# Kernel optimization log

Measured on AMD Instinct MI355X. Metric: run time of the kernel, lower is better.

## Reference

```python
import jax, jax.numpy as jnp
import numpy as np

HEADS = 4
OUT = 64  # hidden_channels


def gat_conv(x, src, dst, N, W, att_src, att_dst, bias):
    # x: [N, Fin] -> h: [N, H, C]
    h = (x @ W).reshape(N, HEADS, OUT)
    a_s = (h * att_src).sum(-1)  # [N, H]
    a_d = (h * att_dst).sum(-1)  # [N, H]
    logits = jax.nn.leaky_relu(a_s[src] + a_d[dst], negative_slope=0.2)  # [E, H]
    # segment softmax over incoming edges of each destination node
    m = jax.ops.segment_max(logits, dst, num_segments=N)
    e = jnp.exp(logits - m[dst])
    z = jax.ops.segment_sum(e, dst, num_segments=N)
    alpha = e / (z[dst] + 1e-16)
    out = jax.ops.segment_sum(h[src] * alpha[:, :, None], dst, num_segments=N)
    return out.reshape(N, HEADS * OUT) + bias


def setup_inputs() -> dict:
    key = jax.random.key(0)
    ks = jax.random.split(key, 16)
    N, E, F = 50000, 800000, 128
    HC = HEADS * OUT  # 256
    s = 0.1
    return {
        "x": jax.random.normal(ks[0], (N, F), jnp.float32),
        "edge_index": jax.random.randint(ks[1], (2, E), 0, N, dtype=jnp.int32),
        "W1": jax.random.normal(ks[2], (F, HC), jnp.float32) * s,
        "as1": jax.random.normal(ks[3], (1, HEADS, OUT), jnp.float32) * s,
        "ad1": jax.random.normal(ks[4], (1, HEADS, OUT), jnp.float32) * s,
        "b1": jnp.zeros((HC,), jnp.float32),
        "W2": jax.random.normal(ks[5], (HC, HC), jnp.float32) * s,
        "as2": jax.random.normal(ks[6], (1, HEADS, OUT), jnp.float32) * s,
        "ad2": jax.random.normal(ks[7], (1, HEADS, OUT), jnp.float32) * s,
        "b2": jnp.zeros((HC,), jnp.float32),
        "lw1": jax.random.normal(ks[8], (HC, OUT), jnp.float32) * s,
        "lb1": jnp.zeros((OUT,), jnp.float32),
        "lw2": jax.random.normal(ks[9], (OUT, 2), jnp.float32) * s,
        "lb2": jnp.zeros((2,), jnp.float32),
    }


def reference(x, edge_index, W1, as1, ad1, b1, W2, as2, ad2, b2, lw1, lb1, lw2, lb2):
    N = x.shape[0]
    # PyG GATConv default add_self_loops=True
    loop = jnp.arange(N, dtype=edge_index.dtype)
    src = jnp.concatenate([edge_index[0], loop])
    dst = jnp.concatenate([edge_index[1], loop])
    h = jax.nn.elu(gat_conv(x, src, dst, N, W1, as1, ad1, b1))
    # dropout is identity at inference
    h = jax.nn.elu(gat_conv(h, src, dst, N, W2, as2, ad2, b2))
    h = jax.nn.relu(h @ lw1 + lb1)
    return jax.nn.log_softmax(h @ lw2 + lb2, axis=1)
```

## Files before the change

kernel.cpp:

```cpp
#include <hip/hip_runtime.h>
#include <math.h>


typedef __attribute__((ext_vector_type(8))) _Float16 half8v;
typedef __attribute__((ext_vector_type(4))) float f32x4;

__device__ __forceinline__ float lrelu(float x) { return x > 0.f ? x : 0.2f * x; }
__device__ __forceinline__ float elu1(float x) { return x > 0.f ? x : (__expf(x) - 1.f); }

__global__ void convert_weights_kernel(const float* __restrict__ W1, const float* __restrict__ W2,
                                       const float* __restrict__ lw1,
                                       _Float16* __restrict__ o1, _Float16* __restrict__ o2,
                                       _Float16* __restrict__ o3, int* __restrict__ indeg,
                                       int N) {
  int t = blockIdx.x * blockDim.x + threadIdx.x;
  if (t < 32768) {
    int n = t >> 7, k = t & 127;
    o1[t] = (_Float16)W1[(long)k * 256 + n];
  } else if (t < 98304) {
    int i = t - 32768;
    int n = i >> 8, k = i & 255;
    o2[i] = (_Float16)W2[(long)k * 256 + n];
  } else if (t < 114688) {
    int i = t - 98304;
    int n = i >> 8, k = i & 255;
    o3[i] = (_Float16)lw1[(long)k * 64 + n];
  } else if (t < 114688 + N) {
    indeg[t - 114688] = 0;
  }
}

__global__ void count_kernel(const int* __restrict__ dst, int E, int* __restrict__ indeg) {
  int e = blockIdx.x * blockDim.x + threadIdx.x;
  if (e < E) atomicAdd(&indeg[dst[e]], 1);
}

__global__ void scan_block_kernel(const int* __restrict__ in, int* __restrict__ incl,
                                  int* __restrict__ bsum, int N) {
  __shared__ int wsum[16];
  int gid = blockIdx.x * 1024 + threadIdx.x;
  int lane = threadIdx.x & 63, w = threadIdx.x >> 6;
  int v = (gid < N) ? in[gid] : 0;
  int sv = v;
#pragma unroll
  for (int o = 1; o < 64; o <<= 1) {
    int t = __shfl_up(sv, o);
    if (lane >= o) sv += t;
  }
  if (lane == 63) wsum[w] = sv;
  __syncthreads();
  if (w == 0) {
    int bs = (lane < 16) ? wsum[lane] : 0;
#pragma unroll
    for (int o = 1; o < 16; o <<= 1) {
      int t = __shfl_up(bs, o);
      if (lane >= o) bs += t;
    }
    if (lane < 16) wsum[lane] = bs;
  }
  __syncthreads();
  if (w > 0) sv += wsum[w - 1];
  if (gid < N) incl[gid] = sv;
  if (threadIdx.x == 1023) bsum[blockIdx.x] = sv;
}

__global__ void scan_finalize_kernel(const int* __restrict__ in, const int* __restrict__ incl,
                                     const int* __restrict__ bsum, int* __restrict__ off,
                                     int* __restrict__ cursor, int N) {
  int gid = blockIdx.x * blockDim.x + threadIdx.x;
  if (gid >= N) return;
  int b = gid >> 10;
  int carry = 0;
  for (int k = 0; k < b; ++k) carry += bsum[k];
  int ic = incl[gid] + carry;
  off[gid + 1] = ic;
  cursor[gid] = ic - in[gid];
  if (gid == 0) off[0] = 0;
}

__global__ void fill_kernel(const int* __restrict__ src, const int* __restrict__ dst, int E,
                            int* __restrict__ cursor, int* __restrict__ csr_src) {
  int e = blockIdx.x * blockDim.x + threadIdx.x;
  if (e < E) {
    int pos = atomicAdd(&cursor[dst[e]], 1);
    csr_src[pos] = src[e];
  }
}

template <typename AT>
__launch_bounds__(256)
__global__ void mfma_gemm_attn_kernel(const AT* __restrict__ A,
                                      const _Float16* __restrict__ B,
                                      const float* __restrict__ att_s,
                                      const float* __restrict__ att_d,
                                      _Float16* __restrict__ C,
                                      float* __restrict__ a_s, float* __restrict__ a_d,
                                      int M, int K) {
  __shared__ _Float16 As[64][40];
  __shared__ _Float16 Bs[2][64][40];
  int tid = threadIdx.x;
  int bm = blockIdx.y * 64, bn = blockIdx.x * 128;
  int lane = tid & 63, wave = tid >> 6;
  int srow = tid >> 2, sch = (tid & 3) * 8;
  const AT* Ap = A + (long)(bm + srow) * K + sch;
  const _Float16* Bp0 = B + (long)(bn + srow) * K + sch;
  const _Float16* Bp1 = B + (long)(bn + 64 + srow) * K + sch;
  bool arow_ok = (bm + srow) < M;
  int fm = lane & 15, fq = lane >> 4;
  f32x4 acc[2][4];
#pragma unroll
  for (int t = 0; t < 2; ++t)
#pragma unroll
    for (int cb = 0; cb < 4; ++cb) acc[t][cb] = (f32x4){0.f, 0.f, 0.f, 0.f};
  for (int k0 = 0; k0 < K; k0 += 32) {
    half8v a8 = {0, 0, 0, 0, 0, 0, 0, 0};
    if (arow_ok) {
      if constexpr (sizeof(AT) == 4) {
        float4 f0 = *(const float4*)(Ap + k0);
        float4 f1 = *(const float4*)(Ap + k0 + 4);
        a8 = (half8v){(_Float16)f0.x, (_Float16)f0.y, (_Float16)f0.z, (_Float16)f0.w,
                      (_Float16)f1.x, (_Float16)f1.y, (_Float16)f1.z, (_Float16)f1.w};
      } else {
        a8 = *(const half8v*)(Ap + k0);
      }
    }
    uint4 vb0 = *(const uint4*)(Bp0 + k0);
    uint4 vb1 = *(const uint4*)(Bp1 + k0);
    *(half8v*)&As[srow][sch] = a8;
    *(uint4*)&Bs[0][srow][sch] = vb0;
    *(uint4*)&Bs[1][srow][sch] = vb1;
    __syncthreads();
    half8v ah = *(const half8v*)&As[wave * 16 + fm][fq * 8];
#pragma unroll
    for (int t = 0; t < 2; ++t)
#pragma unroll
      for (int cb = 0; cb < 4; ++cb) {
        half8v bh = *(const half8v*)&Bs[t][cb * 16 + fm][fq * 8];
        acc[t][cb] = __builtin_amdgcn_mfma_f32_16x16x32_f16(ah, bh, acc[t][cb], 0, 0, 0);
      }
    __syncthreads();
  }
  int row0 = bm + wave * 16 + fq * 4;
#pragma unroll
  for (int t = 0; t < 2; ++t) {
    int headi = blockIdx.x * 2 + t;
    int cbase = bn + t * 64;
    float asv[4], adv[4];
#pragma unroll
    for (int cb = 0; cb < 4; ++cb) {
      int col = cbase + cb * 16 + fm;
      asv[cb] = att_s[col];
      adv[cb] = att_d[col];
    }
#pragma unroll
    for (int r = 0; r < 4; ++r) {
      int row = row0 + r;
      float sp = 0.f, dp = 0.f;
#pragma unroll
      for (int cb = 0; cb < 4; ++cb) {
        float v = acc[t][cb][r];
        sp = fmaf(v, asv[cb], sp);
        dp = fmaf(v, adv[cb], dp);
        if (row < M) C[(long)row * 256 + cbase + cb * 16 + fm] = (_Float16)v;
      }
#pragma unroll
      for (int o = 1; o < 16; o <<= 1) {
        sp += __shfl_xor(sp, o);
        dp += __shfl_xor(dp, o);
      }
      if (fm == 0 && row < M) {
        a_s[(long)row * 4 + headi] = sp;
        a_d[(long)row * 4 + headi] = dp;
      }
    }
  }
}

__launch_bounds__(256)
__global__ void head_mfma_kernel(const _Float16* __restrict__ A, const _Float16* __restrict__ B,
                                 const float* __restrict__ lb1, const float* __restrict__ lw2,
                                 const float* __restrict__ lb2, float* __restrict__ out, int M) {
  __shared__ _Float16 As[64][40];
  __shared__ _Float16 Bs[64][40];
  int tid = threadIdx.x;
  int bm = blockIdx.x * 64;
  int lane = tid & 63, wave = tid >> 6;
  int srow = tid >> 2, sch = (tid & 3) * 8;
  const _Float16* Ap = A + (long)(bm + srow) * 256 + sch;
  const _Float16* Bp = B + (long)srow * 256 + sch;
  int fm = lane & 15, fq = lane >> 4;
  f32x4 acc[4];
#pragma unroll
  for (int cb = 0; cb < 4; ++cb) acc[cb] = (f32x4){0.f, 0.f, 0.f, 0.f};
  for (int k0 = 0; k0 < 256; k0 += 32) {
    uint4 va = *(const uint4*)(Ap + k0);
    uint4 vb = *(const uint4*)(Bp + k0);
    *(uint4*)&As[srow][sch] = va;
    *(uint4*)&Bs[srow][sch] = vb;
    __syncthreads();
    half8v ah = *(const half8v*)&As[wave * 16 + fm][fq * 8];
#pragma unroll
    for (int cb = 0; cb < 4; ++cb) {
      half8v bh = *(const half8v*)&Bs[cb * 16 + fm][fq * 8];
      acc[cb] = __builtin_amdgcn_mfma_f32_16x16x32_f16(ah, bh, acc[cb], 0, 0, 0);
    }
    __syncthreads();
  }
  float lb1c[4], w20[4], w21[4];
#pragma unroll
  for (int cb = 0; cb < 4; ++cb) {
    int col = cb * 16 + fm;
    lb1c[cb] = lb1[col];
    w20[cb] = lw2[col * 2 + 0];
    w21[cb] = lw2[col * 2 + 1];
  }
  float b20 = lb2[0], b21 = lb2[1];
#pragma unroll
  for (int r = 0; r < 4; ++r) {
    float v0 = 0.f, v1 = 0.f;
#pragma unroll
    for (int cb = 0; cb < 4; ++cb) {
      float s = fmaxf(acc[cb][r] + lb1c[cb], 0.f);
      v0 = fmaf(s, w20[cb], v0);
      v1 = fmaf(s, w21[cb], v1);
    }
#pragma unroll
    for (int o = 1; o < 16; o <<= 1) {
      v0 += __shfl_xor(v0, o);
      v1 += __shfl_xor(v1, o);
    }
    if (fm == 0) {
      int row = bm + wave * 16 + fq * 4 + r;
      if (row < M) {
        v0 += b20;
        v1 += b21;
        float mx = fmaxf(v0, v1);
        float ls = mx + logf(expf(v0 - mx) + expf(v1 - mx));
        out[(long)row * 2 + 0] = v0 - ls;
        out[(long)row * 2 + 1] = v1 - ls;
      }
    }
  }
}

__launch_bounds__(256)
__global__ void gat_aggregate8_kernel(const _Float16* __restrict__ h,
                                      const float* __restrict__ a_s,
                                      const float* __restrict__ a_d,
                                      const int* __restrict__ off,
                                      const int* __restrict__ csr_src,
                                      const float* __restrict__ bias,
                                      _Float16* __restrict__ outp, int N) {
  int wid = (blockIdx.x * blockDim.x + threadIdx.x) >> 6;
  int lane = threadIdx.x & 63;
  if (wid >= N) return;
  int c = lane & 31, hlf = lane >> 5, head4 = c >> 3;
  int h1 = lane & 3, sl1 = lane >> 2;
  int beg = off[wid], cnt = off[wid + 1] - beg;
  float ad_h1 = a_d[wid * 4 + h1];
  float m = lrelu(a_s[wid * 4 + h1] + ad_h1);
  float acc[8] = {};
  float z = 0.f;
  if (hlf == 0) {
    z = 1.f;
    half8v sr = *(const half8v*)(h + (long)wid * 256 + c * 8);
#pragma unroll
    for (int i = 0; i < 8; ++i) acc[i] = (float)sr[i];
  }
  for (int c0 = 0; c0 < cnt; c0 += 16) {
    int i2 = c0 + (lane & 15);
    int sv = (i2 < cnt) ? csr_src[beg + i2] : 0;
    int i1 = c0 + sl1;
    int spi = __shfl(sv, sl1);
    float l = (i1 < cnt) ? lrelu(a_s[(long)spi * 4 + h1] + ad_h1) : -1e30f;
    float lm = l;
    lm = fmaxf(lm, __shfl_xor(lm, 4));
    lm = fmaxf(lm, __shfl_xor(lm, 8));
    lm = fmaxf(lm, __shfl_xor(lm, 16));
    lm = fmaxf(lm, __shfl_xor(lm, 32));
    float m_new = fmaxf(m, lm);
    float alpha = __expf(m - m_new);
    float pv = (i1 < cnt) ? __expf(l - m_new) : 0.f;
    m = m_new;
    float alpha4 = __shfl(alpha, head4);
    z *= alpha4;
#pragma unroll
    for (int i = 0; i < 8; ++i) acc[i] *= alpha4;
#pragma unroll 4
    for (int j = 0; j < 16; j += 2) {
      if (c0 + j >= cnt) break;
      int e = j + hlf;
      int s = __shfl(sv, e);
      float p = __shfl(pv, e * 4 + head4);
      z += p;
      half8v rv = *(const half8v*)(h + (long)s * 256 + c * 8);
      acc[0] = fmaf(p, (float)rv[0], acc[0]);
      acc[1] = fmaf(p, (float)rv[1], acc[1]);
      acc[2] = fmaf(p, (float)rv[2], acc[2]);
      acc[3] = fmaf(p, (float)rv[3], acc[3]);
      acc[4] = fmaf(p, (float)rv[4], acc[4]);
      acc[5] = fmaf(p, (float)rv[5], acc[5]);
      acc[6] = fmaf(p, (float)rv[6], acc[6]);
      acc[7] = fmaf(p, (float)rv[7], acc[7]);
    }
  }
  z += __shfl_xor(z, 32);
#pragma unroll
  for (int i = 0; i < 8; ++i) acc[i] += __shfl_xor(acc[i], 32);
  if (hlf == 0) {
    float inv = 1.f / z;
    half8v o;
#pragma unroll
    for (int i = 0; i < 8; ++i) o[i] = (_Float16)elu1(fmaf(acc[i], inv, bias[c * 8 + i]));
    *(half8v*)(outp + (long)wid * 256 + c * 8) = o;
  }
}

static inline int cdiv(int a, int b) { return (a + b - 1) / b; }

extern "C" void kernel_launch(void* const* d_in, const int* in_sizes, int n_in,
                              void* d_out, int out_size, void* d_ws, size_t ws_size,
                              hipStream_t stream) {
  const float* x = (const float*)d_in[0];
  const int* ei = (const int*)d_in[1];
  const float* W1 = (const float*)d_in[2];
  const float* as1 = (const float*)d_in[3];
  const float* ad1 = (const float*)d_in[4];
  const float* b1 = (const float*)d_in[5];
  const float* W2 = (const float*)d_in[6];
  const float* as2 = (const float*)d_in[7];
  const float* ad2 = (const float*)d_in[8];
  const float* b2 = (const float*)d_in[9];
  const float* lw1 = (const float*)d_in[10];
  const float* lb1 = (const float*)d_in[11];
  const float* lw2 = (const float*)d_in[12];
  const float* lb2 = (const float*)d_in[13];
  float* out = (float*)d_out;

  int N = in_sizes[0] / 128;
  int E = in_sizes[1] / 2;
  int Mp = cdiv(N, 64) * 64;

  char* ws = (char*)d_ws;
  _Float16* Wt1 = (_Float16*)ws; ws += 256 * 128 * 2;
  _Float16* Wt2 = (_Float16*)ws; ws += 256 * 256 * 2;
  _Float16* WL = (_Float16*)ws; ws += 64 * 256 * 2;
  _Float16* C = (_Float16*)ws; ws += (size_t)Mp * 256 * 2;
  _Float16* h2 = (_Float16*)ws; ws += (size_t)Mp * 256 * 2;
  float* aS = (float*)ws; ws += (size_t)N * 4 * 4;
  float* aD = (float*)ws; ws += (size_t)N * 4 * 4;
  int* csr_src = (int*)ws; ws += (size_t)E * 4;
  int* indeg = (int*)ws; ws += (size_t)N * 4;
  int* cursor = (int*)ws; ws += (size_t)N * 4;
  int* off = (int*)ws; ws += (size_t)(N + 4) * 4;
  int* incl = (int*)ws; ws += (size_t)N * 4;
  int* bsum = (int*)ws; ws += 64 * 4;

  const int* e_src = ei;
  const int* e_dst = ei + E;
  int nb = cdiv(N, 1024);

  convert_weights_kernel<<<cdiv(114688 + N, 256), 256, 0, stream>>>(W1, W2, lw1, Wt1, Wt2, WL,
                                                                    indeg, N);

  count_kernel<<<cdiv(E, 256), 256, 0, stream>>>(e_dst, E, indeg);
  scan_block_kernel<<<nb, 1024, 0, stream>>>(indeg, incl, bsum, N);
  scan_finalize_kernel<<<cdiv(N, 256), 256, 0, stream>>>(indeg, incl, bsum, off, cursor, N);
  fill_kernel<<<cdiv(E, 256), 256, 0, stream>>>(e_src, e_dst, E, cursor, csr_src);

  mfma_gemm_attn_kernel<float><<<dim3(2, Mp / 64), 256, 0, stream>>>(x, Wt1, as1, ad1, C, aS, aD,
                                                                     N, 128);
  gat_aggregate8_kernel<<<cdiv(N, 4), 256, 0, stream>>>(C, aS, aD, off, csr_src, b1, h2, N);

  mfma_gemm_attn_kernel<_Float16><<<dim3(2, Mp / 64), 256, 0, stream>>>(h2, Wt2, as2, ad2, C, aS,
                                                                        aD, N, 256);
  gat_aggregate8_kernel<<<cdiv(N, 4), 256, 0, stream>>>(C, aS, aD, off, csr_src, b2, h2, N);

  head_mfma_kernel<<<Mp / 64, 256, 0, stream>>>(h2, WL, lb1, lw2, lb2, out, N);
}
```

Baseline: 362.4 us.

## Store features in column-slice blocks and split aggregation into stats and sliced passes

```diff
diff --git a/kernel.cpp b/kernel.cpp
--- a/kernel.cpp
+++ b/kernel.cpp
@@ -95,14 +95,19 @@
                                       const float* __restrict__ att_d,
                                       _Float16* __restrict__ C,
                                       float* __restrict__ a_s, float* __restrict__ a_d,
-                                      int M, int K) {
+                                      int M, int K, int Mp) {
   __shared__ _Float16 As[64][40];
   __shared__ _Float16 Bs[2][64][40];
   int tid = threadIdx.x;
   int bm = blockIdx.y * 64, bn = blockIdx.x * 128;
   int lane = tid & 63, wave = tid >> 6;
   int srow = tid >> 2, sch = (tid & 3) * 8;
-  const AT* Ap = A + (long)(bm + srow) * K + sch;
+  const AT* Ap;
+  if constexpr (sizeof(AT) == 4) {
+    Ap = A + (long)(bm + srow) * K + sch;
+  } else {
+    Ap = A + (long)(bm + srow) * 32 + sch;
+  }
   const _Float16* Bp0 = B + (long)(bn + srow) * K + sch;
   const _Float16* Bp1 = B + (long)(bn + 64 + srow) * K + sch;
   bool arow_ok = (bm + srow) < M;
@@ -121,7 +126,7 @@
         a8 = (half8v){(_Float16)f0.x, (_Float16)f0.y, (_Float16)f0.z, (_Float16)f0.w,
                       (_Float16)f1.x, (_Float16)f1.y, (_Float16)f1.z, (_Float16)f1.w};
       } else {
-        a8 = *(const half8v*)(Ap + k0);
+        a8 = *(const half8v*)(Ap + (long)(k0 >> 5) * Mp * 32);
       }
     }
     uint4 vb0 = *(const uint4*)(Bp0 + k0);
@@ -161,7 +166,10 @@
         float v = acc[t][cb][r];
         sp = fmaf(v, asv[cb], sp);
         dp = fmaf(v, adv[cb], dp);
-        if (row < M) C[(long)row * 256 + cbase + cb * 16 + fm] = (_Float16)v;
+        if (row < M) {
+          int col = cbase + cb * 16 + fm;
+          C[((long)(col >> 5) * Mp + row) * 32 + (col & 31)] = (_Float16)v;
+        }
       }
 #pragma unroll
       for (int o = 1; o < 16; o <<= 1) {
@@ -179,21 +187,22 @@
 __launch_bounds__(256)
 __global__ void head_mfma_kernel(const _Float16* __restrict__ A, const _Float16* __restrict__ B,
                                  const float* __restrict__ lb1, const float* __restrict__ lw2,
-                                 const float* __restrict__ lb2, float* __restrict__ out, int M) {
+                                 const float* __restrict__ lb2, float* __restrict__ out,
+                                 int M, int Mp) {
   __shared__ _Float16 As[64][40];
   __shared__ _Float16 Bs[64][40];
   int tid = threadIdx.x;
   int bm = blockIdx.x * 64;
   int lane = tid & 63, wave = tid >> 6;
   int srow = tid >> 2, sch = (tid & 3) * 8;
-  const _Float16* Ap = A + (long)(bm + srow) * 256 + sch;
+  const _Float16* Ap = A + (long)(bm + srow) * 32 + sch;
   const _Float16* Bp = B + (long)srow * 256 + sch;
   int fm = lane & 15, fq = lane >> 4;
   f32x4 acc[4];
 #pragma unroll
   for (int cb = 0; cb < 4; ++cb) acc[cb] = (f32x4){0.f, 0.f, 0.f, 0.f};
   for (int k0 = 0; k0 < 256; k0 += 32) {
-    uint4 va = *(const uint4*)(Ap + k0);
+    uint4 va = *(const uint4*)(Ap + (long)(k0 >> 5) * Mp * 32);
     uint4 vb = *(const uint4*)(Bp + k0);
     *(uint4*)&As[srow][sch] = va;
     *(uint4*)&Bs[srow][sch] = vb;
@@ -244,75 +253,99 @@
 }
 
 __launch_bounds__(256)
-__global__ void gat_aggregate8_kernel(const _Float16* __restrict__ h,
-                                      const float* __restrict__ a_s,
-                                      const float* __restrict__ a_d,
-                                      const int* __restrict__ off,
-                                      const int* __restrict__ csr_src,
-                                      const float* __restrict__ bias,
-                                      _Float16* __restrict__ outp, int N) {
+__global__ void attn_softmax_stats_kernel(const float* __restrict__ a_s,
+                                          const float* __restrict__ a_d,
+                                          const int* __restrict__ off,
+                                          const int* __restrict__ csr_src,
+                                          float* __restrict__ mOut,
+                                          float* __restrict__ zInvOut, int N) {
   int wid = (blockIdx.x * blockDim.x + threadIdx.x) >> 6;
   int lane = threadIdx.x & 63;
   if (wid >= N) return;
-  int c = lane & 31, hlf = lane >> 5, head4 = c >> 3;
-  int h1 = lane & 3, sl1 = lane >> 2;
+  int h1 = lane & 3, slot = lane >> 2;
   int beg = off[wid], cnt = off[wid + 1] - beg;
   float ad_h1 = a_d[wid * 4 + h1];
   float m = lrelu(a_s[wid * 4 + h1] + ad_h1);
-  float acc[8] = {};
-  float z = 0.f;
-  if (hlf == 0) {
-    z = 1.f;
-    half8v sr = *(const half8v*)(h + (long)wid * 256 + c * 8);
-#pragma unroll
-    for (int i = 0; i < 8; ++i) acc[i] = (float)sr[i];
-  }
+  float z = (slot == 0) ? 1.f : 0.f;
   for (int c0 = 0; c0 < cnt; c0 += 16) {
-    int i2 = c0 + (lane & 15);
-    int sv = (i2 < cnt) ? csr_src[beg + i2] : 0;
-    int i1 = c0 + sl1;
-    int spi = __shfl(sv, sl1);
-    float l = (i1 < cnt) ? lrelu(a_s[(long)spi * 4 + h1] + ad_h1) : -1e30f;
+    int i = c0 + slot;
+    int sv = (i < cnt) ? csr_src[beg + i] : 0;
+    float l = (i < cnt) ? lrelu(a_s[(long)sv * 4 + h1] + ad_h1) : -1e30f;
     float lm = l;
     lm = fmaxf(lm, __shfl_xor(lm, 4));
     lm = fmaxf(lm, __shfl_xor(lm, 8));
     lm = fmaxf(lm, __shfl_xor(lm, 16));
     lm = fmaxf(lm, __shfl_xor(lm, 32));
     float m_new = fmaxf(m, lm);
-    float alpha = __expf(m - m_new);
-    float pv = (i1 < cnt) ? __expf(l - m_new) : 0.f;
+    z *= __expf(m - m_new);
+    z += (i < cnt) ? __expf(l - m_new) : 0.f;
     m = m_new;
-    float alpha4 = __shfl(alpha, head4);
-    z *= alpha4;
-#pragma unroll
-    for (int i = 0; i < 8; ++i) acc[i] *= alpha4;
-#pragma unroll 4
-    for (int j = 0; j < 16; j += 2) {
-      if (c0 + j >= cnt) break;
-      int e = j + hlf;
-      int s = __shfl(sv, e);
-      float p = __shfl(pv, e * 4 + head4);
-      z += p;
-      half8v rv = *(const half8v*)(h + (long)s * 256 + c * 8);
-      acc[0] = fmaf(p, (float)rv[0], acc[0]);
-      acc[1] = fmaf(p, (float)rv[1], acc[1]);
-      acc[2] = fmaf(p, (float)rv[2], acc[2]);
-      acc[3] = fmaf(p, (float)rv[3], acc[3]);
-      acc[4] = fmaf(p, (float)rv[4], acc[4]);
-      acc[5] = fmaf(p, (float)rv[5], acc[5]);
-      acc[6] = fmaf(p, (float)rv[6], acc[6]);
-      acc[7] = fmaf(p, (float)rv[7], acc[7]);
-    }
-  }
+  }
+  z += __shfl_xor(z, 4);
+  z += __shfl_xor(z, 8);
+  z += __shfl_xor(z, 16);
   z += __shfl_xor(z, 32);
-#pragma unroll
-  for (int i = 0; i < 8; ++i) acc[i] += __shfl_xor(acc[i], 32);
-  if (hlf == 0) {
-    float inv = 1.f / z;
+  if (slot == 0) {
+    mOut[(long)h1 * N + wid] = m;
+    zInvOut[(long)h1 * N + wid] = 1.f / (z + 1e-16f);
+  }
+}
+
+__launch_bounds__(256)
+__global__ void gat_aggregate_slice_kernel(const _Float16* __restrict__ hblk,
+                                           const float* __restrict__ a_s,
+                                           const float* __restrict__ a_d,
+                                           const float* __restrict__ mArr,
+                                           const float* __restrict__ zInv,
+                                           const int* __restrict__ off,
+                                           const int* __restrict__ csr_src,
+                                           const float* __restrict__ bias,
+                                           _Float16* __restrict__ outblk,
+                                           int N, int Mp) {
+  int bid = blockIdx.x;
+  int slice = bid & 7;
+  int wid = (bid >> 3) * 4 + (threadIdx.x >> 6);
+  int lane = threadIdx.x & 63;
+  if (wid >= N) return;
+  int colg = lane & 3, slot = lane >> 2;
+  int hb = slice >> 1;
+  const _Float16* hs = hblk + (long)slice * Mp * 32;
+  int beg = off[wid], cnt = off[wid + 1] - beg;
+  float m = mArr[(long)hb * N + wid];
+  float inv = zInv[(long)hb * N + wid];
+  float ad_hb = a_d[wid * 4 + hb];
+  float acc[8] = {};
+  if (slot == 0) {
+    float lself = lrelu(a_s[wid * 4 + hb] + ad_hb);
+    float p = __expf(lself - m);
+    half8v sr = *(const half8v*)(hs + (long)wid * 32 + colg * 8);
+#pragma unroll
+    for (int j = 0; j < 8; ++j) acc[j] = p * (float)sr[j];
+  }
+  for (int c0 = 0; c0 < cnt; c0 += 16) {
+    int i = c0 + slot;
+    if (i < cnt) {
+      int sv = csr_src[beg + i];
+      float l = lrelu(a_s[(long)sv * 4 + hb] + ad_hb);
+      float p = __expf(l - m);
+      half8v rv = *(const half8v*)(hs + (long)sv * 32 + colg * 8);
+#pragma unroll
+      for (int j = 0; j < 8; ++j) acc[j] = fmaf(p, (float)rv[j], acc[j]);
+    }
+  }
+#pragma unroll
+  for (int j = 0; j < 8; ++j) {
+    acc[j] += __shfl_xor(acc[j], 4);
+    acc[j] += __shfl_xor(acc[j], 8);
+    acc[j] += __shfl_xor(acc[j], 16);
+    acc[j] += __shfl_xor(acc[j], 32);
+  }
+  if (slot == 0) {
+    int cbase = slice * 32 + colg * 8;
     half8v o;
 #pragma unroll
-    for (int i = 0; i < 8; ++i) o[i] = (_Float16)elu1(fmaf(acc[i], inv, bias[c * 8 + i]));
-    *(half8v*)(outp + (long)wid * 256 + c * 8) = o;
+    for (int j = 0; j < 8; ++j) o[j] = (_Float16)elu1(fmaf(acc[j], inv, bias[cbase + j]));
+    *(half8v*)(outblk + (long)slice * Mp * 32 + (long)wid * 32 + colg * 8) = o;
   }
 }
 
@@ -349,6 +382,8 @@
   _Float16* h2 = (_Float16*)ws; ws += (size_t)Mp * 256 * 2;
   float* aS = (float*)ws; ws += (size_t)N * 4 * 4;
   float* aD = (float*)ws; ws += (size_t)N * 4 * 4;
+  float* mArr = (float*)ws; ws += (size_t)N * 4 * 4;
+  float* zInv = (float*)ws; ws += (size_t)N * 4 * 4;
   int* csr_src = (int*)ws; ws += (size_t)E * 4;
   int* indeg = (int*)ws; ws += (size_t)N * 4;
   int* cursor = (int*)ws; ws += (size_t)N * 4;
@@ -369,12 +404,16 @@
   fill_kernel<<<cdiv(E, 256), 256, 0, stream>>>(e_src, e_dst, E, cursor, csr_src);
 
   mfma_gemm_attn_kernel<float><<<dim3(2, Mp / 64), 256, 0, stream>>>(x, Wt1, as1, ad1, C, aS, aD,
-                                                                     N, 128);
-  gat_aggregate8_kernel<<<cdiv(N, 4), 256, 0, stream>>>(C, aS, aD, off, csr_src, b1, h2, N);
+                                                                     N, 128, Mp);
+  attn_softmax_stats_kernel<<<cdiv(N, 4), 256, 0, stream>>>(aS, aD, off, csr_src, mArr, zInv, N);
+  gat_aggregate_slice_kernel<<<8 * cdiv(N, 4), 256, 0, stream>>>(C, aS, aD, mArr, zInv, off,
+                                                                 csr_src, b1, h2, N, Mp);
 
   mfma_gemm_attn_kernel<_Float16><<<dim3(2, Mp / 64), 256, 0, stream>>>(h2, Wt2, as2, ad2, C, aS,
-                                                                        aD, N, 256);
-  gat_aggregate8_kernel<<<cdiv(N, 4), 256, 0, stream>>>(C, aS, aD, off, csr_src, b2, h2, N);
-
-  head_mfma_kernel<<<Mp / 64, 256, 0, stream>>>(h2, WL, lb1, lw2, lb2, out, N);
-}
+                                                                        aD, N, 256, Mp);
+  attn_softmax_stats_kernel<<<cdiv(N, 4), 256, 0, stream>>>(aS, aD, off, csr_src, mArr, zInv, N);
+  gat_aggregate_slice_kernel<<<8 * cdiv(N, 4), 256, 0, stream>>>(C, aS, aD, mArr, zInv, off,
+                                                                 csr_src, b2, h2, N, Mp);
+
+  head_mfma_kernel<<<Mp / 64, 256, 0, stream>>>(h2, WL, lb1, lw2, lb2, out, N, Mp);
+}
```

Measured after the change: 574.7 us. +58.6%, slower.

## Split GAT aggregation into softmax-stats pass and weighted-gather pass

Applied to the files above, without the earlier changes.

```diff
diff --git a/kernel.cpp b/kernel.cpp
--- a/kernel.cpp
+++ b/kernel.cpp
@@ -244,55 +244,88 @@
 }
 
 __launch_bounds__(256)
-__global__ void gat_aggregate8_kernel(const _Float16* __restrict__ h,
-                                      const float* __restrict__ a_s,
-                                      const float* __restrict__ a_d,
-                                      const int* __restrict__ off,
-                                      const int* __restrict__ csr_src,
-                                      const float* __restrict__ bias,
-                                      _Float16* __restrict__ outp, int N) {
+__global__ void attn_softmax_stats_kernel(const float* __restrict__ a_s,
+                                          const float* __restrict__ a_d,
+                                          const int* __restrict__ off,
+                                          const int* __restrict__ csr_src,
+                                          float* __restrict__ mOut,
+                                          float* __restrict__ zInvOut,
+                                          float* __restrict__ alphaE, int N) {
   int wid = (blockIdx.x * blockDim.x + threadIdx.x) >> 6;
   int lane = threadIdx.x & 63;
   if (wid >= N) return;
-  int c = lane & 31, hlf = lane >> 5, head4 = c >> 3;
-  int h1 = lane & 3, sl1 = lane >> 2;
+  int h1 = lane & 3, slot = lane >> 2;
   int beg = off[wid], cnt = off[wid + 1] - beg;
   float ad_h1 = a_d[wid * 4 + h1];
   float m = lrelu(a_s[wid * 4 + h1] + ad_h1);
-  float acc[8] = {};
-  float z = 0.f;
-  if (hlf == 0) {
-    z = 1.f;
-    half8v sr = *(const half8v*)(h + (long)wid * 256 + c * 8);
-#pragma unroll
-    for (int i = 0; i < 8; ++i) acc[i] = (float)sr[i];
-  }
+  float z = (slot == 0) ? 1.f : 0.f;
   for (int c0 = 0; c0 < cnt; c0 += 16) {
-    int i2 = c0 + (lane & 15);
-    int sv = (i2 < cnt) ? csr_src[beg + i2] : 0;
-    int i1 = c0 + sl1;
-    int spi = __shfl(sv, sl1);
-    float l = (i1 < cnt) ? lrelu(a_s[(long)spi * 4 + h1] + ad_h1) : -1e30f;
+    int i = c0 + slot;
+    int sv = (i < cnt) ? csr_src[beg + i] : 0;
+    float l = (i < cnt) ? lrelu(a_s[(long)sv * 4 + h1] + ad_h1) : -1e30f;
     float lm = l;
     lm = fmaxf(lm, __shfl_xor(lm, 4));
     lm = fmaxf(lm, __shfl_xor(lm, 8));
     lm = fmaxf(lm, __shfl_xor(lm, 16));
     lm = fmaxf(lm, __shfl_xor(lm, 32));
     float m_new = fmaxf(m, lm);
-    float alpha = __expf(m - m_new);
-    float pv = (i1 < cnt) ? __expf(l - m_new) : 0.f;
+    z *= __expf(m - m_new);
+    z += (i < cnt) ? __expf(l - m_new) : 0.f;
     m = m_new;
-    float alpha4 = __shfl(alpha, head4);
-    z *= alpha4;
-#pragma unroll
-    for (int i = 0; i < 8; ++i) acc[i] *= alpha4;
+  }
+  z += __shfl_xor(z, 4);
+  z += __shfl_xor(z, 8);
+  z += __shfl_xor(z, 16);
+  z += __shfl_xor(z, 32);
+  if (slot == 0) {
+    mOut[(long)wid * 4 + h1] = m;
+    zInvOut[(long)wid * 4 + h1] = 1.f / (z + 1e-16f);
+  }
+  for (int c0 = 0; c0 < cnt; c0 += 16) {
+    int i = c0 + slot;
+    if (i < cnt) {
+      int sv = csr_src[beg + i];
+      float l = lrelu(a_s[(long)sv * 4 + h1] + ad_h1);
+      alphaE[(long)(beg + i) * 4 + h1] = __expf(l - m);
+    }
+  }
+}
+
+__launch_bounds__(256)
+__global__ void gat_aggregate_pre_kernel(const _Float16* __restrict__ h,
+                                         const float* __restrict__ alphaE,
+                                         const float* __restrict__ a_s,
+                                         const float* __restrict__ a_d,
+                                         const float* __restrict__ mArr,
+                                         const float* __restrict__ zInv,
+                                         const int* __restrict__ off,
+                                         const int* __restrict__ csr_src,
+                                         const float* __restrict__ bias,
+                                         _Float16* __restrict__ outp, int N) {
+  int wid = (blockIdx.x * blockDim.x + threadIdx.x) >> 6;
+  int lane = threadIdx.x & 63;
+  if (wid >= N) return;
+  int c = lane & 31, hlf = lane >> 5, head4 = c >> 3;
+  int beg = off[wid], cnt = off[wid + 1] - beg;
+  float m = mArr[(long)wid * 4 + head4];
+  float inv = zInv[(long)wid * 4 + head4];
+  float acc[8] = {};
+  if (hlf == 0) {
+    float pself = __expf(lrelu(a_s[(long)wid * 4 + head4] + a_d[(long)wid * 4 + head4]) - m);
+    half8v sr = *(const half8v*)(h + (long)wid * 256 + c * 8);
+#pragma unroll
+    for (int i = 0; i < 8; ++i) acc[i] = pself * (float)sr[i];
+  }
+  const float* ap = alphaE + (long)beg * 4;
+  for (int c0 = 0; c0 < cnt; c0 += 16) {
+    int i2 = c0 + (lane & 15);
+    int sv = (i2 < cnt) ? csr_src[beg + i2] : 0;
 #pragma unroll 4
     for (int j = 0; j < 16; j += 2) {
       if (c0 + j >= cnt) break;
       int e = j + hlf;
       int s = __shfl(sv, e);
-      float p = __shfl(pv, e * 4 + head4);
-      z += p;
+      float p = (c0 + e < cnt) ? ap[(long)(c0 + e) * 4 + head4] : 0.f;
       half8v rv = *(const half8v*)(h + (long)s * 256 + c * 8);
       acc[0] = fmaf(p, (float)rv[0], acc[0]);
       acc[1] = fmaf(p, (float)rv[1], acc[1]);
@@ -304,11 +337,9 @@
       acc[7] = fmaf(p, (float)rv[7], acc[7]);
     }
   }
-  z += __shfl_xor(z, 32);
 #pragma unroll
   for (int i = 0; i < 8; ++i) acc[i] += __shfl_xor(acc[i], 32);
   if (hlf == 0) {
-    float inv = 1.f / z;
     half8v o;
 #pragma unroll
     for (int i = 0; i < 8; ++i) o[i] = (_Float16)elu1(fmaf(acc[i], inv, bias[c * 8 + i]));
@@ -349,6 +380,9 @@
   _Float16* h2 = (_Float16*)ws; ws += (size_t)Mp * 256 * 2;
   float* aS = (float*)ws; ws += (size_t)N * 4 * 4;
   float* aD = (float*)ws; ws += (size_t)N * 4 * 4;
+  float* mArr = (float*)ws; ws += (size_t)N * 4 * 4;
+  float* zInv = (float*)ws; ws += (size_t)N * 4 * 4;
+  float* alphaE = (float*)ws; ws += (size_t)E * 4 * 4;
   int* csr_src = (int*)ws; ws += (size_t)E * 4;
   int* indeg = (int*)ws; ws += (size_t)N * 4;
   int* cursor = (int*)ws; ws += (size_t)N * 4;
@@ -370,11 +404,17 @@
 
   mfma_gemm_attn_kernel<float><<<dim3(2, Mp / 64), 256, 0, stream>>>(x, Wt1, as1, ad1, C, aS, aD,
                                                                      N, 128);
-  gat_aggregate8_kernel<<<cdiv(N, 4), 256, 0, stream>>>(C, aS, aD, off, csr_src, b1, h2, N);
+  attn_softmax_stats_kernel<<<cdiv(N, 4), 256, 0, stream>>>(aS, aD, off, csr_src, mArr, zInv,
+                                                            alphaE, N);
+  gat_aggregate_pre_kernel<<<cdiv(N, 4), 256, 0, stream>>>(C, alphaE, aS, aD, mArr, zInv, off,
+                                                           csr_src, b1, h2, N);
 
   mfma_gemm_attn_kernel<_Float16><<<dim3(2, Mp / 64), 256, 0, stream>>>(h2, Wt2, as2, ad2, C, aS,
                                                                         aD, N, 256);
-  gat_aggregate8_kernel<<<cdiv(N, 4), 256, 0, stream>>>(C, aS, aD, off, csr_src, b2, h2, N);
+  attn_softmax_stats_kernel<<<cdiv(N, 4), 256, 0, stream>>>(aS, aD, off, csr_src, mArr, zInv,
+                                                            alphaE, N);
+  gat_aggregate_pre_kernel<<<cdiv(N, 4), 256, 0, stream>>>(C, alphaE, aS, aD, mArr, zInv, off,
+                                                           csr_src, b2, h2, N);
 
   head_mfma_kernel<<<Mp / 64, 256, 0, stream>>>(h2, WL, lb1, lw2, lb2, out, N);
 }
```

New measurement: 407.1 us. 12.3% more time.

## Drop online softmax max tracking and batch gather loads in GAT aggregation

Applied to the files above, without the earlier changes.

```diff
diff --git a/kernel.cpp b/kernel.cpp
--- a/kernel.cpp
+++ b/kernel.cpp
@@ -244,13 +244,13 @@
 }
 
 __launch_bounds__(256)
-__global__ void gat_aggregate8_kernel(const _Float16* __restrict__ h,
-                                      const float* __restrict__ a_s,
-                                      const float* __restrict__ a_d,
-                                      const int* __restrict__ off,
-                                      const int* __restrict__ csr_src,
-                                      const float* __restrict__ bias,
-                                      _Float16* __restrict__ outp, int N) {
+__global__ void gat_aggregate_exp_kernel(const _Float16* __restrict__ h,
+                                         const float* __restrict__ a_s,
+                                         const float* __restrict__ a_d,
+                                         const int* __restrict__ off,
+                                         const int* __restrict__ csr_src,
+                                         const float* __restrict__ bias,
+                                         _Float16* __restrict__ outp, int N) {
   int wid = (blockIdx.x * blockDim.x + threadIdx.x) >> 6;
   int lane = threadIdx.x & 63;
   if (wid >= N) return;
@@ -258,37 +258,72 @@
   int h1 = lane & 3, sl1 = lane >> 2;
   int beg = off[wid], cnt = off[wid + 1] - beg;
   float ad_h1 = a_d[wid * 4 + h1];
-  float m = lrelu(a_s[wid * 4 + h1] + ad_h1);
+  float psl = __expf(lrelu(a_s[wid * 4 + h1] + ad_h1));
+  float pself = __shfl(psl, head4);
+  float z = 0.f;
   float acc[8] = {};
-  float z = 0.f;
   if (hlf == 0) {
-    z = 1.f;
+    z = pself;
     half8v sr = *(const half8v*)(h + (long)wid * 256 + c * 8);
 #pragma unroll
-    for (int i = 0; i < 8; ++i) acc[i] = (float)sr[i];
-  }
-  for (int c0 = 0; c0 < cnt; c0 += 16) {
-    int i2 = c0 + (lane & 15);
+    for (int i = 0; i < 8; ++i) acc[i] = pself * (float)sr[i];
+  }
+  int nfull = cnt & ~15;
+  for (int c0 = 0; c0 < nfull; c0 += 16) {
+    int sv = csr_src[beg + c0 + (lane & 15)];
+    half8v rv0, rv1, rv2, rv3, rv4, rv5, rv6, rv7;
+    {
+      int s0 = __shfl(sv, 0 + hlf);
+      int s1 = __shfl(sv, 2 + hlf);
+      int s2 = __shfl(sv, 4 + hlf);
+      int s3 = __shfl(sv, 6 + hlf);
+      int s4 = __shfl(sv, 8 + hlf);
+      int s5 = __shfl(sv, 10 + hlf);
+      int s6 = __shfl(sv, 12 + hlf);
+      int s7 = __shfl(sv, 14 + hlf);
+      rv0 = *(const half8v*)(h + (long)s0 * 256 + c * 8);
+      rv1 = *(const half8v*)(h + (long)s1 * 256 + c * 8);
+      rv2 = *(const half8v*)(h + (long)s2 * 256 + c * 8);
+      rv3 = *(const half8v*)(h + (long)s3 * 256 + c * 8);
+      rv4 = *(const half8v*)(h + (long)s4 * 256 + c * 8);
+      rv5 = *(const half8v*)(h + (long)s5 * 256 + c * 8);
+      rv6 = *(const half8v*)(h + (long)s6 * 256 + c * 8);
+      rv7 = *(const half8v*)(h + (long)s7 * 256 + c * 8);
+    }
+    int spi = __shfl(sv, sl1);
+    float pv = __expf(lrelu(a_s[(long)spi * 4 + h1] + ad_h1));
+#define AGG_STEP(J, RV)                                             \
+    {                                                               \
+      float p = __shfl(pv, (2 * (J) + hlf) * 4 + head4);            \
+      z += p;                                                       \
+      acc[0] = fmaf(p, (float)RV[0], acc[0]);                       \
+      acc[1] = fmaf(p, (float)RV[1], acc[1]);                       \
+      acc[2] = fmaf(p, (float)RV[2], acc[2]);                       \
+      acc[3] = fmaf(p, (float)RV[3], acc[3]);                       \
+      acc[4] = fmaf(p, (float)RV[4], acc[4]);                       \
+      acc[5] = fmaf(p, (float)RV[5], acc[5]);                       \
+      acc[6] = fmaf(p, (float)RV[6], acc[6]);                       \
+      acc[7] = fmaf(p, (float)RV[7], acc[7]);                       \
+    }
+    AGG_STEP(0, rv0)
+    AGG_STEP(1, rv1)
+    AGG_STEP(2, rv2)
+    AGG_STEP(3, rv3)
+    AGG_STEP(4, rv4)
+    AGG_STEP(5, rv5)
+    AGG_STEP(6, rv6)
+    AGG_STEP(7, rv7)
+#undef AGG_STEP
+  }
+  if (nfull < cnt) {
+    int i2 = nfull + (lane & 15);
     int sv = (i2 < cnt) ? csr_src[beg + i2] : 0;
-    int i1 = c0 + sl1;
+    int i1 = nfull + sl1;
     int spi = __shfl(sv, sl1);
-    float l = (i1 < cnt) ? lrelu(a_s[(long)spi * 4 + h1] + ad_h1) : -1e30f;
-    float lm = l;
-    lm = fmaxf(lm, __shfl_xor(lm, 4));
-    lm = fmaxf(lm, __shfl_xor(lm, 8));
-    lm = fmaxf(lm, __shfl_xor(lm, 16));
-    lm = fmaxf(lm, __shfl_xor(lm, 32));
-    float m_new = fmaxf(m, lm);
-    float alpha = __expf(m - m_new);
-    float pv = (i1 < cnt) ? __expf(l - m_new) : 0.f;
-    m = m_new;
-    float alpha4 = __shfl(alpha, head4);
-    z *= alpha4;
-#pragma unroll
-    for (int i = 0; i < 8; ++i) acc[i] *= alpha4;
+    float pv = (i1 < cnt) ? __expf(lrelu(a_s[(long)spi * 4 + h1] + ad_h1)) : 0.f;
 #pragma unroll 4
     for (int j = 0; j < 16; j += 2) {
-      if (c0 + j >= cnt) break;
+      if (nfull + j >= cnt) break;
       int e = j + hlf;
       int s = __shfl(sv, e);
       float p = __shfl(pv, e * 4 + head4);
@@ -370,11 +405,11 @@
 
   mfma_gemm_attn_kernel<float><<<dim3(2, Mp / 64), 256, 0, stream>>>(x, Wt1, as1, ad1, C, aS, aD,
                                                                      N, 128);
-  gat_aggregate8_kernel<<<cdiv(N, 4), 256, 0, stream>>>(C, aS, aD, off, csr_src, b1, h2, N);
+  gat_aggregate_exp_kernel<<<cdiv(N, 4), 256, 0, stream>>>(C, aS, aD, off, csr_src, b1, h2, N);
 
   mfma_gemm_attn_kernel<_Float16><<<dim3(2, Mp / 64), 256, 0, stream>>>(h2, Wt2, as2, ad2, C, aS,
                                                                         aD, N, 256);
-  gat_aggregate8_kernel<<<cdiv(N, 4), 256, 0, stream>>>(C, aS, aD, off, csr_src, b2, h2, N);
+  gat_aggregate_exp_kernel<<<cdiv(N, 4), 256, 0, stream>>>(C, aS, aD, off, csr_src, b2, h2, N);
 
   head_mfma_kernel<<<Mp / 64, 256, 0, stream>>>(h2, WL, lb1, lw2, lb2, out, N);
 }
```

New measurement: 380.9 us. +5.1%, slower.
